# Kernel optimization log

Hardware: AMD Instinct MI355X
Metric: run time of the kernel (lower is better)

## Reference

```python
import jax, jax.numpy as jnp
import numpy as np

N = 50000
E = 800000
D_IN = 256
D_OUT = 256
ALPHA = 0.5


def setup_inputs() -> dict:
    key = jax.random.key(0)
    k1, k2, k3, k4, k5, k6 = jax.random.split(key, 6)
    stdv = 1.0 / np.sqrt(D_OUT)
    return {
        "input": jax.random.normal(k1, (N, D_IN), dtype=jnp.float32),
        "adj_src": jax.random.randint(k2, (E,), 0, N, dtype=jnp.int64),
        "adj_dst": jax.random.randint(k3, (E,), 0, N, dtype=jnp.int64),
        "adj_w": jax.random.uniform(k4, (E,), dtype=jnp.float32),
        "init_input": jax.random.normal(k5, (N, D_OUT), dtype=jnp.float32),
        "weight": jax.random.uniform(k6, (D_IN, D_OUT), dtype=jnp.float32,
                                     minval=-stdv, maxval=stdv),
    }


def reference(input, adj_src, adj_dst, adj_w, init_input, weight):
    # support = input @ W          [N, D_OUT] (dense GEMM)
    support = jnp.matmul(input, weight)
    # spmm: out[dst] += w * support[src]   (COO aggregate)
    msgs = support[adj_src] * adj_w[:, None]          # [E, D_OUT]
    agg = jax.ops.segment_sum(msgs, adj_dst, num_segments=N)  # [N, D_OUT]
    # alpha-blended residual + ReLU (bias=False, act=ReLU)
    out = agg * ALPHA + init_input * (1.0 - ALPHA)
    return jax.nn.relu(out)
```

## Files before the change

kernel.cpp:

```cpp
#include <hip/hip_runtime.h>

#define ALPHA 0.5f

typedef short short8v __attribute__((ext_vector_type(8)));
typedef float f32x4 __attribute__((ext_vector_type(4)));

__device__ __forceinline__ unsigned short f2bf(float f) {
  union { float f; unsigned u; } v; v.f = f;
  unsigned r = v.u + 0x7FFFu + ((v.u >> 16) & 1u);
  return (unsigned short)(r >> 16);
}
__device__ __forceinline__ float bf2f(unsigned short u) {
  union { unsigned u; float f; } v; v.u = ((unsigned)u) << 16;
  return v.f;
}

__global__ void transpose_w(const float* __restrict__ W, unsigned short* __restrict__ Wt) {
  __shared__ float tile[16][17];
  int kb = blockIdx.x * 16, nb = blockIdx.y * 16;
  tile[threadIdx.y][threadIdx.x] = W[(kb + threadIdx.y) * 256 + nb + threadIdx.x];
  __syncthreads();
  Wt[(nb + threadIdx.y) * 256 + kb + threadIdx.x] = f2bf(tile[threadIdx.x][threadIdx.y]);
}

__global__ __launch_bounds__(256) void gemm_mfma(
    const float* __restrict__ A, const unsigned short* __restrict__ Wt,
    unsigned short* __restrict__ C, int M) {
  __shared__ char smem[2][16384];
  const int tid = threadIdx.x;
  const int lane = tid & 63;
  const int w = tid >> 6;
  const int wm = w >> 1, wn = w & 1;
  const int row0 = blockIdx.x * 128, col0 = blockIdx.y * 128;

  f32x4 acc[4][4];
  #pragma unroll
  for (int m = 0; m < 4; ++m)
    #pragma unroll
    for (int n = 0; n < 4; ++n) acc[m][n] = (f32x4){0.f, 0.f, 0.f, 0.f};

  const int aR = tid >> 1;
  const int aKs = (tid & 1) * 16;
  const int aRow = (row0 + aR < M) ? (row0 + aR) : (M - 1);
  const float* aP = A + (size_t)aRow * 256 + aKs;
  const int aWrOff = (aR >> 4) * 1024 + (aKs >> 3) * 256 + (aR & 15) * 16;

  int cur = 0;
  {
    float4 av[4];
    #pragma unroll
    for (int j = 0; j < 4; ++j) av[j] = *reinterpret_cast<const float4*>(aP + j * 4);
    #pragma unroll
    for (int i = 0; i < 2; ++i) {
      int s = w * 2 + i;
      const unsigned short* g = Wt + (size_t)(col0 + s * 16 + (lane & 15)) * 256 + (lane >> 4) * 8;
      __builtin_amdgcn_global_load_lds(
          (const __attribute__((address_space(1))) void*)g,
          (__attribute__((address_space(3))) void*)(&smem[0][8192 + s * 1024]),
          16, 0, 0);
    }
    unsigned short ab[16];
    #pragma unroll
    for (int j = 0; j < 4; ++j) {
      ab[j * 4 + 0] = f2bf(av[j].x); ab[j * 4 + 1] = f2bf(av[j].y);
      ab[j * 4 + 2] = f2bf(av[j].z); ab[j * 4 + 3] = f2bf(av[j].w);
    }
    *reinterpret_cast<short8v*>(&smem[0][aWrOff])       = *reinterpret_cast<short8v*>(&ab[0]);
    *reinterpret_cast<short8v*>(&smem[0][aWrOff + 256]) = *reinterpret_cast<short8v*>(&ab[8]);
    __syncthreads();
  }

  #pragma unroll
  for (int t = 0; t < 8; ++t) {
    float4 av[4];
    const bool pf = (t < 7);
    if (pf) {
      const int k0 = (t + 1) * 32;
      #pragma unroll
      for (int j = 0; j < 4; ++j) av[j] = *reinterpret_cast<const float4*>(aP + k0 + j * 4);
      #pragma unroll
      for (int i = 0; i < 2; ++i) {
        int s = w * 2 + i;
        const unsigned short* g = Wt + (size_t)(col0 + s * 16 + (lane & 15)) * 256 + k0 + (lane >> 4) * 8;
        __builtin_amdgcn_global_load_lds(
            (const __attribute__((address_space(1))) void*)g,
            (__attribute__((address_space(3))) void*)(&smem[cur ^ 1][8192 + s * 1024]),
            16, 0, 0);
      }
    }
    short8v af[4], bf[4];
    #pragma unroll
    for (int m = 0; m < 4; ++m)
      af[m] = *reinterpret_cast<const short8v*>(&smem[cur][(wm * 4 + m) * 1024 + lane * 16]);
    #pragma unroll
    for (int n = 0; n < 4; ++n)
      bf[n] = *reinterpret_cast<const short8v*>(&smem[cur][8192 + (wn * 4 + n) * 1024 + lane * 16]);
    #pragma unroll
    for (int m = 0; m < 4; ++m)
      #pragma unroll
      for (int n = 0; n < 4; ++n)
        acc[m][n] = __builtin_amdgcn_mfma_f32_16x16x32_bf16(af[m], bf[n], acc[m][n], 0, 0, 0);
    if (pf) {
      unsigned short ab[16];
      #pragma unroll
      for (int j = 0; j < 4; ++j) {
        ab[j * 4 + 0] = f2bf(av[j].x); ab[j * 4 + 1] = f2bf(av[j].y);
        ab[j * 4 + 2] = f2bf(av[j].z); ab[j * 4 + 3] = f2bf(av[j].w);
      }
      *reinterpret_cast<short8v*>(&smem[cur ^ 1][aWrOff])       = *reinterpret_cast<short8v*>(&ab[0]);
      *reinterpret_cast<short8v*>(&smem[cur ^ 1][aWrOff + 256]) = *reinterpret_cast<short8v*>(&ab[8]);
    }
    __syncthreads();
    cur ^= 1;
  }

  #pragma unroll
  for (int m = 0; m < 4; ++m) {
    #pragma unroll
    for (int n = 0; n < 4; ++n) {
      const int col = col0 + wn * 64 + n * 16 + (lane & 15);
      #pragma unroll
      for (int r = 0; r < 4; ++r) {
        const int row = row0 + wm * 64 + m * 16 + (lane >> 4) * 4 + r;
        if (row < M) C[(size_t)row * 256 + col] = f2bf(acc[m][n][r]);
      }
    }
  }
}

__global__ void histogram_dst(const int* __restrict__ dst, int* __restrict__ deg, int E) {
  int i = blockIdx.x * blockDim.x + threadIdx.x;
  if (i < E) atomicAdd(&deg[dst[i]], 1);
}

__global__ __launch_bounds__(256) void scan_pass1(const int* __restrict__ deg,
                                                  int* __restrict__ excl,
                                                  int* __restrict__ partial, int N) {
  const int tid = threadIdx.x;
  const int base = blockIdx.x * 1024 + tid * 4;
  int4 v = make_int4(0, 0, 0, 0);
  if (base + 3 < N) v = *reinterpret_cast<const int4*>(&deg[base]);
  else {
    if (base + 0 < N) v.x = deg[base + 0];
    if (base + 1 < N) v.y = deg[base + 1];
    if (base + 2 < N) v.z = deg[base + 2];
  }
  const int s = v.x + v.y + v.z + v.w;
  const int lane = tid & 63, wid = tid >> 6;
  int ps = s;
  #pragma unroll
  for (int off = 1; off < 64; off <<= 1) {
    int t = __shfl_up(ps, off, 64);
    if (lane >= off) ps += t;
  }
  __shared__ int wsum[4];
  if (lane == 63) wsum[wid] = ps;
  __syncthreads();
  int woff = 0;
  #pragma unroll
  for (int w2 = 0; w2 < 4; ++w2) woff += (w2 < wid) ? wsum[w2] : 0;
  const int texcl = woff + ps - s;
  int4 e = make_int4(texcl, texcl + v.x, texcl + v.x + v.y, texcl + v.x + v.y + v.z);
  if (base + 3 < N) *reinterpret_cast<int4*>(&excl[base]) = e;
  else {
    if (base + 0 < N) excl[base + 0] = e.x;
    if (base + 1 < N) excl[base + 1] = e.y;
    if (base + 2 < N) excl[base + 2] = e.z;
  }
  if (tid == 255) partial[blockIdx.x] = woff + ps;
}

__global__ __launch_bounds__(256) void scan_pass2(const int* __restrict__ excl,
                                                  const int* __restrict__ partial,
                                                  int* __restrict__ row_ptr,
                                                  int* __restrict__ cursor, int N, int NB) {
  __shared__ int s_off;
  const int tid = threadIdx.x;
  if (tid < 64) {
    int v = (tid < NB && tid < (int)blockIdx.x) ? partial[tid] : 0;
    #pragma unroll
    for (int off = 1; off < 64; off <<= 1) v += __shfl_xor(v, off, 64);
    if (tid == 0) s_off = v;
  }
  __syncthreads();
  const int off = s_off;
  const int base = blockIdx.x * 1024 + tid * 4;
  if (base + 3 < N) {
    int4 v = *reinterpret_cast<const int4*>(&excl[base]);
    v.x += off; v.y += off; v.z += off; v.w += off;
    *reinterpret_cast<int4*>(&row_ptr[base]) = v;
    *reinterpret_cast<int4*>(&cursor[base]) = v;
  } else {
    for (int j = 0; j < 4; ++j)
      if (base + j < N) { int v = excl[base + j] + off; row_ptr[base + j] = v; cursor[base + j] = v; }
  }
}

__global__ void reindex_edges(const int* __restrict__ src, const int* __restrict__ dst,
                              const float* __restrict__ w, int* __restrict__ cursor,
                              int2* __restrict__ edges, int E) {
  int i = blockIdx.x * blockDim.x + threadIdx.x;
  if (i < E) {
    int d = dst[i];
    int slot = atomicAdd(&cursor[d], 1);
    edges[slot] = make_int2(src[i], __float_as_int(w[i] * ALPHA));
  }
}

__global__ __launch_bounds__(256) void aggregate(
    const unsigned short* __restrict__ support,
    const int* __restrict__ row_ptr, const int* __restrict__ deg,
    const int2* __restrict__ edges,
    const float* __restrict__ init, float* __restrict__ out, int N) {
  int node = blockIdx.x * 4 + (threadIdx.x >> 6);
  if (node >= N) return;
  int lane = threadIdx.x & 63;
  int start = row_ptr[node], cnt = deg[node];

  float4 acc = make_float4(0.f, 0.f, 0.f, 0.f);
  int e = 0;
  for (; e + 3 < cnt; e += 4) {
    int2 e0 = edges[start + e + 0], e1 = edges[start + e + 1];
    int2 e2 = edges[start + e + 2], e3 = edges[start + e + 3];
    ushort4 v0 = *reinterpret_cast<const ushort4*>(&support[(size_t)e0.x * 256 + lane * 4]);
    ushort4 v1 = *reinterpret_cast<const ushort4*>(&support[(size_t)e1.x * 256 + lane * 4]);
    ushort4 v2 = *reinterpret_cast<const ushort4*>(&support[(size_t)e2.x * 256 + lane * 4]);
    ushort4 v3 = *reinterpret_cast<const ushort4*>(&support[(size_t)e3.x * 256 + lane * 4]);
    float w0 = __int_as_float(e0.y), w1 = __int_as_float(e1.y);
    float w2 = __int_as_float(e2.y), w3 = __int_as_float(e3.y);
    acc.x += w0 * bf2f(v0.x) + w1 * bf2f(v1.x) + w2 * bf2f(v2.x) + w3 * bf2f(v3.x);
    acc.y += w0 * bf2f(v0.y) + w1 * bf2f(v1.y) + w2 * bf2f(v2.y) + w3 * bf2f(v3.y);
    acc.z += w0 * bf2f(v0.z) + w1 * bf2f(v1.z) + w2 * bf2f(v2.z) + w3 * bf2f(v3.z);
    acc.w += w0 * bf2f(v0.w) + w1 * bf2f(v1.w) + w2 * bf2f(v2.w) + w3 * bf2f(v3.w);
  }
  for (; e < cnt; ++e) {
    int2 e0 = edges[start + e];
    ushort4 v0 = *reinterpret_cast<const ushort4*>(&support[(size_t)e0.x * 256 + lane * 4]);
    float w0 = __int_as_float(e0.y);
    acc.x += w0 * bf2f(v0.x); acc.y += w0 * bf2f(v0.y);
    acc.z += w0 * bf2f(v0.z); acc.w += w0 * bf2f(v0.w);
  }
  float4 ini = *reinterpret_cast<const float4*>(&init[(size_t)node * 256 + lane * 4]);
  float4 o;
  o.x = fmaxf(acc.x + (1.f - ALPHA) * ini.x, 0.f);
  o.y = fmaxf(acc.y + (1.f - ALPHA) * ini.y, 0.f);
  o.z = fmaxf(acc.z + (1.f - ALPHA) * ini.z, 0.f);
  o.w = fmaxf(acc.w + (1.f - ALPHA) * ini.w, 0.f);
  *reinterpret_cast<float4*>(&out[(size_t)node * 256 + lane * 4]) = o;
}

extern "C" void kernel_launch(void* const* d_in, const int* in_sizes, int n_in,
                              void* d_out, int out_size, void* d_ws, size_t ws_size,
                              hipStream_t stream) {
  const float* input   = (const float*)d_in[0];
  const int*   adj_src = (const int*)d_in[1];
  const int*   adj_dst = (const int*)d_in[2];
  const float* adj_w   = (const float*)d_in[3];
  const float* init_in = (const float*)d_in[4];
  const float* weight  = (const float*)d_in[5];
  float* out = (float*)d_out;

  const int N = in_sizes[0] / 256;
  const int E = in_sizes[1];

  char* ws = (char*)d_ws;
  unsigned short* support = (unsigned short*)ws; ws += (size_t)N * 256 * 2;
  unsigned short* Wt      = (unsigned short*)ws; ws += 256 * 256 * 2;
  int* deg     = (int*)ws; ws += (size_t)N * 4;
  int* row_ptr = (int*)ws; ws += (size_t)N * 4;
  int* cursor  = (int*)ws; ws += (size_t)N * 4;
  int* excl    = (int*)ws; ws += (size_t)N * 4;
  int* partial = (int*)ws; ws += 256;
  int2* edges  = (int2*)ws; ws += (size_t)E * 8;

  const int NB = (N + 1023) / 1024;

  transpose_w<<<dim3(16, 16), dim3(16, 16), 0, stream>>>(weight, Wt);
  gemm_mfma<<<dim3((N + 127) / 128, 2), 256, 0, stream>>>(input, Wt, support, N);

  hipMemsetAsync(deg, 0, (size_t)N * 4, stream);
  histogram_dst<<<(E + 255) / 256, 256, 0, stream>>>(adj_dst, deg, E);
  scan_pass1<<<NB, 256, 0, stream>>>(deg, excl, partial, N);
  scan_pass2<<<NB, 256, 0, stream>>>(excl, partial, row_ptr, cursor, N, NB);
  reindex_edges<<<(E + 255) / 256, 256, 0, stream>>>(adj_src, adj_dst, adj_w, cursor, edges, E);

  aggregate<<<(N + 3) / 4, 256, 0, stream>>>(support, row_ptr, deg, edges, init_in, out, N);
}
```

Baseline: 192.8 us.

## Use full-width GEMM tiles and pack edges into 32-bit src+fp16 weight

The GEMM now computes all 256 output columns per block, so each block reads its rows of the fp32 input only once instead of twice, at the cost of doubling the accumulator registers per thread. Edge records are packed into one 32-bit word holding the source index shifted left by 15 and a truncated fp16 weight, which halves edge-list traffic in reindexing and aggregation. The aggregate loop is unrolled to 8 edges to keep more gathers in flight, and the init load is hoisted ahead of the loop. Weight precision drops to fp16 with the lowest mantissa bit dropped, and source indices must fit in 17 bits, which holds for N=50000.

```diff
diff --git a/kernel.cpp b/kernel.cpp
--- a/kernel.cpp
+++ b/kernel.cpp
@@ -1,4 +1,5 @@
 #include <hip/hip_runtime.h>
+#include <hip/hip_fp16.h>
 
 #define ALPHA 0.5f
 
@@ -26,18 +27,18 @@
 __global__ __launch_bounds__(256) void gemm_mfma(
     const float* __restrict__ A, const unsigned short* __restrict__ Wt,
     unsigned short* __restrict__ C, int M) {
-  __shared__ char smem[2][16384];
+  __shared__ char smem[2][24576];
   const int tid = threadIdx.x;
   const int lane = tid & 63;
   const int w = tid >> 6;
   const int wm = w >> 1, wn = w & 1;
-  const int row0 = blockIdx.x * 128, col0 = blockIdx.y * 128;
-
-  f32x4 acc[4][4];
+  const int row0 = blockIdx.x * 128;
+
+  f32x4 acc[4][8];
   #pragma unroll
   for (int m = 0; m < 4; ++m)
     #pragma unroll
-    for (int n = 0; n < 4; ++n) acc[m][n] = (f32x4){0.f, 0.f, 0.f, 0.f};
+    for (int n = 0; n < 8; ++n) acc[m][n] = (f32x4){0.f, 0.f, 0.f, 0.f};
 
   const int aR = tid >> 1;
   const int aKs = (tid & 1) * 16;
@@ -51,9 +52,9 @@
     #pragma unroll
     for (int j = 0; j < 4; ++j) av[j] = *reinterpret_cast<const float4*>(aP + j * 4);
     #pragma unroll
-    for (int i = 0; i < 2; ++i) {
-      int s = w * 2 + i;
-      const unsigned short* g = Wt + (size_t)(col0 + s * 16 + (lane & 15)) * 256 + (lane >> 4) * 8;
+    for (int i = 0; i < 4; ++i) {
+      int s = w * 4 + i;
+      const unsigned short* g = Wt + (size_t)(s * 16 + (lane & 15)) * 256 + (lane >> 4) * 8;
       __builtin_amdgcn_global_load_lds(
           (const __attribute__((address_space(1))) void*)g,
           (__attribute__((address_space(3))) void*)(&smem[0][8192 + s * 1024]),
@@ -79,27 +80,27 @@
       #pragma unroll
       for (int j = 0; j < 4; ++j) av[j] = *reinterpret_cast<const float4*>(aP + k0 + j * 4);
       #pragma unroll
-      for (int i = 0; i < 2; ++i) {
-        int s = w * 2 + i;
-        const unsigned short* g = Wt + (size_t)(col0 + s * 16 + (lane & 15)) * 256 + k0 + (lane >> 4) * 8;
+      for (int i = 0; i < 4; ++i) {
+        int s = w * 4 + i;
+        const unsigned short* g = Wt + (size_t)(s * 16 + (lane & 15)) * 256 + k0 + (lane >> 4) * 8;
         __builtin_amdgcn_global_load_lds(
             (const __attribute__((address_space(1))) void*)g,
             (__attribute__((address_space(3))) void*)(&smem[cur ^ 1][8192 + s * 1024]),
             16, 0, 0);
       }
     }
-    short8v af[4], bf[4];
+    short8v af[4], bfv[8];
     #pragma unroll
     for (int m = 0; m < 4; ++m)
       af[m] = *reinterpret_cast<const short8v*>(&smem[cur][(wm * 4 + m) * 1024 + lane * 16]);
     #pragma unroll
-    for (int n = 0; n < 4; ++n)
-      bf[n] = *reinterpret_cast<const short8v*>(&smem[cur][8192 + (wn * 4 + n) * 1024 + lane * 16]);
+    for (int n = 0; n < 8; ++n)
+      bfv[n] = *reinterpret_cast<const short8v*>(&smem[cur][8192 + (wn * 8 + n) * 1024 + lane * 16]);
     #pragma unroll
     for (int m = 0; m < 4; ++m)
       #pragma unroll
-      for (int n = 0; n < 4; ++n)
-        acc[m][n] = __builtin_amdgcn_mfma_f32_16x16x32_bf16(af[m], bf[n], acc[m][n], 0, 0, 0);
+      for (int n = 0; n < 8; ++n)
+        acc[m][n] = __builtin_amdgcn_mfma_f32_16x16x32_bf16(af[m], bfv[n], acc[m][n], 0, 0, 0);
     if (pf) {
       unsigned short ab[16];
       #pragma unroll
@@ -117,8 +118,8 @@
   #pragma unroll
   for (int m = 0; m < 4; ++m) {
     #pragma unroll
-    for (int n = 0; n < 4; ++n) {
-      const int col = col0 + wn * 64 + n * 16 + (lane & 15);
+    for (int n = 0; n < 8; ++n) {
+      const int col = wn * 128 + n * 16 + (lane & 15);
       #pragma unroll
       for (int r = 0; r < 4; ++r) {
         const int row = row0 + wm * 64 + m * 16 + (lane >> 4) * 4 + r;
@@ -198,49 +199,58 @@
 
 __global__ void reindex_edges(const int* __restrict__ src, const int* __restrict__ dst,
                               const float* __restrict__ w, int* __restrict__ cursor,
-                              int2* __restrict__ edges, int E) {
+                              unsigned* __restrict__ edges, int E) {
   int i = blockIdx.x * blockDim.x + threadIdx.x;
   if (i < E) {
     int d = dst[i];
     int slot = atomicAdd(&cursor[d], 1);
-    edges[slot] = make_int2(src[i], __float_as_int(w[i] * ALPHA));
-  }
+    unsigned hb = __half_as_ushort(__float2half(w[i] * ALPHA));
+    edges[slot] = ((unsigned)src[i] << 15) | (hb >> 1);
+  }
+}
+
+__device__ __forceinline__ float unpack_w(unsigned p) {
+  return __half2float(__ushort_as_half((unsigned short)((p & 0x7FFFu) << 1)));
 }
 
 __global__ __launch_bounds__(256) void aggregate(
     const unsigned short* __restrict__ support,
     const int* __restrict__ row_ptr, const int* __restrict__ deg,
-    const int2* __restrict__ edges,
+    const unsigned* __restrict__ edges,
     const float* __restrict__ init, float* __restrict__ out, int N) {
   int node = blockIdx.x * 4 + (threadIdx.x >> 6);
   if (node >= N) return;
   int lane = threadIdx.x & 63;
   int start = row_ptr[node], cnt = deg[node];
 
+  float4 ini = *reinterpret_cast<const float4*>(&init[(size_t)node * 256 + lane * 4]);
+
   float4 acc = make_float4(0.f, 0.f, 0.f, 0.f);
   int e = 0;
-  for (; e + 3 < cnt; e += 4) {
-    int2 e0 = edges[start + e + 0], e1 = edges[start + e + 1];
-    int2 e2 = edges[start + e + 2], e3 = edges[start + e + 3];
-    ushort4 v0 = *reinterpret_cast<const ushort4*>(&support[(size_t)e0.x * 256 + lane * 4]);
-    ushort4 v1 = *reinterpret_cast<const ushort4*>(&support[(size_t)e1.x * 256 + lane * 4]);
-    ushort4 v2 = *reinterpret_cast<const ushort4*>(&support[(size_t)e2.x * 256 + lane * 4]);
-    ushort4 v3 = *reinterpret_cast<const ushort4*>(&support[(size_t)e3.x * 256 + lane * 4]);
-    float w0 = __int_as_float(e0.y), w1 = __int_as_float(e1.y);
-    float w2 = __int_as_float(e2.y), w3 = __int_as_float(e3.y);
-    acc.x += w0 * bf2f(v0.x) + w1 * bf2f(v1.x) + w2 * bf2f(v2.x) + w3 * bf2f(v3.x);
-    acc.y += w0 * bf2f(v0.y) + w1 * bf2f(v1.y) + w2 * bf2f(v2.y) + w3 * bf2f(v3.y);
-    acc.z += w0 * bf2f(v0.z) + w1 * bf2f(v1.z) + w2 * bf2f(v2.z) + w3 * bf2f(v3.z);
-    acc.w += w0 * bf2f(v0.w) + w1 * bf2f(v1.w) + w2 * bf2f(v2.w) + w3 * bf2f(v3.w);
+  for (; e + 7 < cnt; e += 8) {
+    unsigned p[8];
+    #pragma unroll
+    for (int j = 0; j < 8; ++j) p[j] = edges[start + e + j];
+    ushort4 v[8];
+    #pragma unroll
+    for (int j = 0; j < 8; ++j)
+      v[j] = *reinterpret_cast<const ushort4*>(&support[(size_t)(p[j] >> 15) * 256 + lane * 4]);
+    #pragma unroll
+    for (int j = 0; j < 8; ++j) {
+      float wj = unpack_w(p[j]);
+      acc.x += wj * bf2f(v[j].x);
+      acc.y += wj * bf2f(v[j].y);
+      acc.z += wj * bf2f(v[j].z);
+      acc.w += wj * bf2f(v[j].w);
+    }
   }
   for (; e < cnt; ++e) {
-    int2 e0 = edges[start + e];
-    ushort4 v0 = *reinterpret_cast<const ushort4*>(&support[(size_t)e0.x * 256 + lane * 4]);
-    float w0 = __int_as_float(e0.y);
-    acc.x += w0 * bf2f(v0.x); acc.y += w0 * bf2f(v0.y);
-    acc.z += w0 * bf2f(v0.z); acc.w += w0 * bf2f(v0.w);
-  }
-  float4 ini = *reinterpret_cast<const float4*>(&init[(size_t)node * 256 + lane * 4]);
+    unsigned p = edges[start + e];
+    ushort4 v = *reinterpret_cast<const ushort4*>(&support[(size_t)(p >> 15) * 256 + lane * 4]);
+    float wj = unpack_w(p);
+    acc.x += wj * bf2f(v.x); acc.y += wj * bf2f(v.y);
+    acc.z += wj * bf2f(v.z); acc.w += wj * bf2f(v.w);
+  }
   float4 o;
   o.x = fmaxf(acc.x + (1.f - ALPHA) * ini.x, 0.f);
   o.y = fmaxf(acc.y + (1.f - ALPHA) * ini.y, 0.f);
@@ -271,12 +281,12 @@
   int* cursor  = (int*)ws; ws += (size_t)N * 4;
   int* excl    = (int*)ws; ws += (size_t)N * 4;
   int* partial = (int*)ws; ws += 256;
-  int2* edges  = (int2*)ws; ws += (size_t)E * 8;
+  unsigned* edges = (unsigned*)ws; ws += (size_t)E * 4;
 
   const int NB = (N + 1023) / 1024;
 
   transpose_w<<<dim3(16, 16), dim3(16, 16), 0, stream>>>(weight, Wt);
-  gemm_mfma<<<dim3((N + 127) / 128, 2), 256, 0, stream>>>(input, Wt, support, N);
+  gemm_mfma<<<dim3((N + 127) / 128), 256, 0, stream>>>(input, Wt, support, N);
 
   hipMemsetAsync(deg, 0, (size_t)N * 4, stream);
   histogram_dst<<<(E + 255) / 256, 256, 0, stream>>>(adj_dst, deg, E);
```

New measurement: 191.8 us. No clear change (-0.5%).
